# Optimization experiments

Hardware: AMD Instinct MI355X
Metric: run time of the kernel (lower is better)

## Reference

```python
import jax, jax.numpy as jnp
import numpy as np

EPS = 1e-5       # BatchNorm2d eps
NHEAD = 8
FILL = -1e30     # stands in for scores_fill_value=-inf (finite for grad safety)


def _proj(x, w, b, g, beta, mean, var):
    # Conv2d 1x1 over NCHW (H=1) == channel matmul, followed by eval-mode BatchNorm2d.
    y = jnp.einsum('oc,bcht->boht', w, x) + b[None, :, None, None]
    inv = g * jax.lax.rsqrt(var + EPS)
    return y * inv[None, :, None, None] + (beta - mean * inv)[None, :, None, None]


def setup_inputs() -> dict:
    rng = jax.random.key(0)
    ks = jax.random.split(rng, 10)
    B, C, T = 8, 512, 1024
    query = jax.random.normal(ks[0], (B, C, 1, T), jnp.float32)
    key = jax.random.normal(ks[1], (B, C, 1, T), jnp.float32)
    value = jax.random.normal(ks[2], (B, C, 1, T), jnp.float32)
    mask = jax.random.randint(ks[3], (B, 1, T, T), 0, 2).astype(jnp.int32)
    Ws = jax.random.normal(ks[4], (4, C, C), jnp.float32) * (1.0 / np.sqrt(C))
    bs = jax.random.normal(ks[5], (4, C), jnp.float32) * 0.1
    gammas = jax.random.uniform(ks[6], (4, C), jnp.float32, 0.5, 1.5)
    betas = jax.random.normal(ks[7], (4, C), jnp.float32) * 0.1
    means = jax.random.normal(ks[8], (4, C), jnp.float32) * 0.1
    vars_ = jax.random.uniform(ks[9], (4, C), jnp.float32, 0.5, 1.5)
    return dict(query=query, key=key, value=value, mask=mask, Ws=Ws, bs=bs,
                gammas=gammas, betas=betas, means=means, vars_=vars_)


def reference(query, key, value, mask, Ws, bs, gammas, betas, means, vars_):
    B, C, _, T1 = query.shape
    T2 = key.shape[3]
    h = NHEAD
    d_k = C // h
    denom = 1.0 / np.sqrt(d_k)

    q = _proj(query, Ws[0], bs[0], gammas[0], betas[0], means[0], vars_[0]).reshape(B, h, d_k, T1)
    k = _proj(key,   Ws[1], bs[1], gammas[1], betas[1], means[1], vars_[1]).reshape(B, h, d_k, T2)
    v = _proj(value, Ws[2], bs[2], gammas[2], betas[2], means[2], vars_[2]).reshape(B, h, d_k, T2)

    # scores = k^T @ q -> (B, h, T2, T1); softmax over key axis (dim=2, matching torch)
    scores = jnp.einsum('bhds,bhdt->bhst', k, q) * denom
    mask0 = jnp.transpose(mask, (0, 1, 3, 2)) == 0  # (B, 1, T2, T1)
    scores = jnp.where(mask0, FILL, scores)
    attn = jax.nn.softmax(scores, axis=2)
    attn = jnp.where(mask0, 0.0, attn)

    # x = v @ attn -> (B, h, d_k, T1) -> (B, C, 1, T1)
    x = jnp.einsum('bhds,bhst->bhdt', v, attn).reshape(B, C, 1, T1)
    out = _proj(x, Ws[3], bs[3], gammas[3], betas[3], means[3], vars_[3])

    # cache=None branch: new_cache = cat(raw key, raw value) along channel dim
    new_cache = jnp.concatenate([key, value], axis=1)
    return (out, new_cache)
```

## Files before the change

kernel.cpp:

```cpp
#include <hip/hip_runtime.h>

typedef unsigned short u16;
typedef unsigned int   u32;
typedef short  bfrag   __attribute__((ext_vector_type(8)));
typedef float  accfrag __attribute__((ext_vector_type(16)));
typedef unsigned int   u32x4 __attribute__((ext_vector_type(4)));
typedef unsigned short u16x4 __attribute__((ext_vector_type(4)));
typedef float          f32x4 __attribute__((ext_vector_type(4)));

#define B_SZ 8
#define C_SZ 512
#define T_SZ 1024
#define NH   8
#define DK   64

#define QSCL 0.18033688f

__device__ __forceinline__ u16 f2bf(float f) {
  u32 u = __float_as_uint(f);
  u = u + 0x7fffu + ((u >> 16) & 1u);
  return (u16)(u >> 16);
}

__device__ __forceinline__ float fexp2(float x) {
  return __builtin_amdgcn_exp2f(x);
}

__device__ __forceinline__ u32 cvtpk(float lo, float hi) {
  u32 r;
  asm("v_cvt_pk_bf16_f32 %0, %1, %2" : "=v"(r) : "v"(lo), "v"(hi));
  return r;
}

__device__ __forceinline__ void permswap(u32 &a, u32 &b) {
  asm volatile("v_permlane32_swap_b32 %0, %1" : "+v"(a), "+v"(b));
}

__device__ __forceinline__ void gload16(const u16* g, u16* l) {
  __builtin_amdgcn_global_load_lds(
      (const __attribute__((address_space(1))) void*)g,
      (__attribute__((address_space(3))) void*)l, 16, 0, 0);
}

__global__ void prep_w(const float* __restrict__ Ws, const float* __restrict__ gam,
                       const float* __restrict__ var, u16* __restrict__ Wp) {
  int idx = blockIdx.x * 256 + threadIdx.x;
  int io = idx >> 9;
  float inv = gam[io] * rsqrtf(var[io] + 1e-5f);
  Wp[idx] = f2bf(Ws[idx] * inv);
}

__global__ void prep_b(const float* __restrict__ bs, const float* __restrict__ gam,
                       const float* __restrict__ beta, const float* __restrict__ mean,
                       const float* __restrict__ var, float* __restrict__ bp) {
  int idx = blockIdx.x * 256 + threadIdx.x;
  float inv = gam[idx] * rsqrtf(var[idx] + 1e-5f);
  bp[idx] = bs[idx] * inv + beta[idx] - mean[idx] * inv;
}

__global__ void transpose_cvt(const float* __restrict__ q, const float* __restrict__ k,
                              const float* __restrict__ v, u16* __restrict__ Xt,
                              float* __restrict__ cache) {
  __shared__ float tile[32][33];
  int z = blockIdx.z;
  int src = z >> 3, b = z & 7;
  const float* in = (src == 0) ? q : ((src == 1) ? k : v);
  u16* out = Xt + (size_t)src * ((size_t)B_SZ * T_SZ * C_SZ);
  int t0 = blockIdx.x * 32, c0 = blockIdx.y * 32;
  int tx = threadIdx.x & 31, ty = threadIdx.x >> 5;
#pragma unroll
  for (int rr = 0; rr < 4; ++rr) {
    int c = c0 + ty + rr * 8;
    float val = in[(((size_t)b * C_SZ + c) << 10) + t0 + tx];
    tile[ty + rr * 8][tx] = val;
    if (src >= 1) {
      int cc = c + (src == 2 ? 512 : 0);
      cache[((size_t)b << 20) + ((size_t)cc << 10) + t0 + tx] = val;
    }
  }
  __syncthreads();
#pragma unroll
  for (int rr = 0; rr < 4; ++rr) {
    int t = t0 + ty + rr * 8;
    out[(((size_t)b << 10) + t) * C_SZ + c0 + tx] = f2bf(tile[tx][ty + rr * 8]);
  }
}

__global__ void mask_bits(const int* __restrict__ mask, u32* __restrict__ mbT) {
  int w = blockIdx.x * 256 + threadIdx.x;
  int bt = w >> 5;
  int st = w & 31;
  const int* mrow = mask + ((size_t)bt << 10) + (st << 5);
  u32 word = 0;
#pragma unroll
  for (int j = 0; j < 32; j += 4) {
    int4 m4 = *(const int4*)(mrow + j);
    word |= (m4.x != 0 ? 1u : 0u) << j;
    word |= (m4.y != 0 ? 1u : 0u) << (j + 1);
    word |= (m4.z != 0 ? 1u : 0u) << (j + 2);
    word |= (m4.w != 0 ? 1u : 0u) << (j + 3);
  }
  int b = bt >> 10, t = bt & 1023;
  mbT[(((size_t)b * 32 + st) << 10) + t] = word;
}

__launch_bounds__(256, 2)
__global__ void gemm_qkv(const u16* __restrict__ Wp, const float* __restrict__ bpA,
                         const u16* __restrict__ Xt,
                         u16* __restrict__ Qf, u16* __restrict__ Kf, u16* __restrict__ Vf) {
  __shared__ __align__(16) u16 lds[2 * 128 * 64];
  int tid = threadIdx.x;
  int src = blockIdx.z >> 3;
  int b   = blockIdx.z & 7;
  int t0 = blockIdx.x * 128;
  int o0 = blockIdx.y * 128;
  int wid = tid >> 6, lane = tid & 63;
  int ln = lane & 31, hi = lane >> 5;
  int wr = wid >> 1, wc = wid & 1;

  const u16* Wsrc = Wp + (size_t)src * 262144;
  const float* bp = bpA + src * 512;
  const u16* Xin  = Xt + (size_t)src * ((size_t)B_SZ * T_SZ * C_SZ);
  u16* Yout = (src == 0) ? Qf : (src == 1 ? Kf : Vf);

  const char* Ag = (const char*)Wsrc;
  const char* Bg = (const char*)(Xin + (((size_t)b << 10) + t0) * C_SZ);
  char* ldsA = (char*)lds;
  char* ldsB = (char*)lds + 16384;

  accfrag acc[2][2];
#pragma unroll
  for (int m2 = 0; m2 < 2; ++m2)
#pragma unroll
    for (int n2 = 0; n2 < 2; ++n2)
#pragma unroll
      for (int e = 0; e < 16; ++e) acc[m2][n2][e] = 0.f;

  int lin = tid * 16;
  for (int kt = 0; kt < 8; ++kt) {
    u32x4 ra[4], rb[4];
#pragma unroll
    for (int it = 0; it < 4; ++it) {
      int off = lin + it * 4096;
      int r = off >> 7, cb = off & 127;
      ra[it] = *(const u32x4*)(Ag + (size_t)(o0 + r) * 1024 + kt * 128 + cb);
      rb[it] = *(const u32x4*)(Bg + (size_t)r * 1024 + kt * 128 + cb);
    }
    __syncthreads();
#pragma unroll
    for (int it = 0; it < 4; ++it) {
      int off = lin + it * 4096;
      *(u32x4*)(ldsA + off) = ra[it];
      *(u32x4*)(ldsB + off) = rb[it];
    }
    __syncthreads();
#pragma unroll
    for (int kk = 0; kk < 4; ++kk) {
      bfrag a[2], bb[2];
#pragma unroll
      for (int m2 = 0; m2 < 2; ++m2)
        a[m2] = *(const bfrag*)(ldsA + (wr * 64 + m2 * 32 + ln) * 128 + kk * 32 + hi * 16);
#pragma unroll
      for (int n2 = 0; n2 < 2; ++n2)
        bb[n2] = *(const bfrag*)(ldsB + (wc * 64 + n2 * 32 + ln) * 128 + kk * 32 + hi * 16);
#pragma unroll
      for (int m2 = 0; m2 < 2; ++m2)
#pragma unroll
        for (int n2 = 0; n2 < 2; ++n2)
          acc[m2][n2] = __builtin_amdgcn_mfma_f32_32x32x16_bf16(a[m2], bb[n2], acc[m2][n2], 0, 0, 0);
    }
  }

  float oscl = (src == 0) ? QSCL : 1.0f;
#pragma unroll
  for (int m2 = 0; m2 < 2; ++m2) {
    int obase = o0 + wr * 64 + m2 * 32;
#pragma unroll
    for (int n2 = 0; n2 < 2; ++n2) {
      int t = t0 + wc * 64 + n2 * 32 + ln;
      if (src < 2) {
        int tt5 = t & 31, st = t >> 5;
#pragma unroll
        for (int g = 0; g < 4; ++g) {
          int d0 = obase + 8 * g + 4 * hi;
          int hh = d0 >> 6, dd = d0 & 63;
          u16x4 pk4;
#pragma unroll
          for (int qq = 0; qq < 4; ++qq)
            pk4[qq] = f2bf((acc[m2][n2][4 * g + qq] + bp[d0 + qq]) * oscl);
          size_t a = ((((size_t)b * 8 + hh) * 32 + st) << 11)
                   + (size_t)((dd >> 4) * 512 + (tt5 + 32 * ((dd >> 3) & 1)) * 8 + (dd & 7));
          *(u16x4*)(Yout + a) = pk4;
        }
      } else {
        int s = t, st = s >> 5;
#pragma unroll
        for (int r = 0; r < 16; ++r) {
          int d = obase + (r & 3) + 8 * (r >> 2) + 4 * hi;
          int hh = d >> 6, dd = d & 63;
          int fi = ((s >> 4) & 1) * 2 + ((dd >> 5) & 1);
          int l  = (dd & 31) + ((s >> 3) & 1) * 32;
          Yout[((((size_t)b * 8 + hh) * 32 + st) << 11)
               + (size_t)(fi * 512 + l * 8 + (s & 7))] = f2bf(acc[m2][n2][r] + bp[d]);
        }
      }
    }
  }
}

__launch_bounds__(256, 2)
__global__ void gemm_out(const u16* __restrict__ Wp, const float* __restrict__ bp,
                         const u16* __restrict__ Xin, float* __restrict__ Yout) {
  __shared__ __align__(16) u16 lds[2 * 128 * 64];
  int tid = threadIdx.x;
  int b  = blockIdx.z;
  int t0 = blockIdx.x * 128;
  int o0 = blockIdx.y * 128;
  int wid = tid >> 6, lane = tid & 63;
  int ln = lane & 31, hi = lane >> 5;
  int wr = wid >> 1, wc = wid & 1;

  const char* Ag = (const char*)Wp;
  const char* Bg = (const char*)(Xin + (((size_t)b << 10) + t0) * C_SZ);
  char* ldsA = (char*)lds;
  char* ldsB = (char*)lds + 16384;

  accfrag acc[2][2];
#pragma unroll
  for (int m2 = 0; m2 < 2; ++m2)
#pragma unroll
    for (int n2 = 0; n2 < 2; ++n2)
#pragma unroll
      for (int e = 0; e < 16; ++e) acc[m2][n2][e] = 0.f;

  int lin = tid * 16;
  for (int kt = 0; kt < 8; ++kt) {
    u32x4 ra[4], rb[4];
#pragma unroll
    for (int it = 0; it < 4; ++it) {
      int off = lin + it * 4096;
      int r = off >> 7, cb = off & 127;
      ra[it] = *(const u32x4*)(Ag + (size_t)(o0 + r) * 1024 + kt * 128 + cb);
      rb[it] = *(const u32x4*)(Bg + (size_t)r * 1024 + kt * 128 + cb);
    }
    __syncthreads();
#pragma unroll
    for (int it = 0; it < 4; ++it) {
      int off = lin + it * 4096;
      *(u32x4*)(ldsA + off) = ra[it];
      *(u32x4*)(ldsB + off) = rb[it];
    }
    __syncthreads();
#pragma unroll
    for (int kk = 0; kk < 4; ++kk) {
      bfrag a[2], bb[2];
#pragma unroll
      for (int m2 = 0; m2 < 2; ++m2)
        a[m2] = *(const bfrag*)(ldsA + (wr * 64 + m2 * 32 + ln) * 128 + kk * 32 + hi * 16);
#pragma unroll
      for (int n2 = 0; n2 < 2; ++n2)
        bb[n2] = *(const bfrag*)(ldsB + (wc * 64 + n2 * 32 + ln) * 128 + kk * 32 + hi * 16);
#pragma unroll
      for (int m2 = 0; m2 < 2; ++m2)
#pragma unroll
        for (int n2 = 0; n2 < 2; ++n2)
          acc[m2][n2] = __builtin_amdgcn_mfma_f32_32x32x16_bf16(a[m2], bb[n2], acc[m2][n2], 0, 0, 0);
    }
  }

#pragma unroll
  for (int m2 = 0; m2 < 2; ++m2) {
    int obase = o0 + wr * 64 + m2 * 32;
#pragma unroll
    for (int n2 = 0; n2 < 2; ++n2) {
      int t = t0 + wc * 64 + n2 * 32 + ln;
#pragma unroll
      for (int r = 0; r < 16; ++r) {
        int o = obase + (r & 3) + 8 * (r >> 2) + 4 * hi;
        Yout[(((size_t)b * C_SZ + o) << 10) + t] = acc[m2][n2][r] + bp[o];
      }
    }
  }
}

__launch_bounds__(512, 4)
__global__ void attn_fused(const u16* __restrict__ Qf, const u16* __restrict__ Kf,
                           const u16* __restrict__ Vf, const u32* __restrict__ mbT,
                           u16* __restrict__ X2) {
  __shared__ __align__(16) char smem[33 * 1024];
  u16*   sK   = (u16*)smem;
  u16*   sV   = (u16*)(smem + 16384);
  float* comb = (float*)smem;
  float* mlb  = (float*)(smem + 32768);

  int n = blockIdx.x;
  int bh = n & 63, tb = n >> 6;
  int b = bh >> 3, h = bh & 7;
  int tid = threadIdx.x;
  int wid = tid >> 6, lane = tid & 63;
  int grp = wid >> 2, wl = wid & 3;
  int ln = lane & 31, hi = lane >> 5;
  int tt = tb * 4 + wl;
  int t  = tt * 32 + ln;

  const u16* QfT = Qf + (((size_t)bh * 32 + tt) << 11);
  bfrag qf[4];
#pragma unroll
  for (int j = 0; j < 4; ++j)
    qf[j] = *(const bfrag*)(QfT + j * 512 + lane * 8);

  const u16* KfB = Kf + ((size_t)bh << 16);
  const u16* VfB = Vf + ((size_t)bh << 16);
  const u32* mcol = mbT + ((size_t)b << 15) + t;

  float m_run = -1.0e4f, l_run = 0.f;
  accfrag accd[2];
#pragma unroll
  for (int m2 = 0; m2 < 2; ++m2)
#pragma unroll
    for (int e = 0; e < 16; ++e) accd[m2][e] = 0.f;

  int gtid = tid & 255;
  int soff = gtid * 8;
  u16* sKg = sK + grp * 4096;
  u16* sVg = sV + grp * 4096;
  int st0 = grp * 16;

  gload16(KfB + ((size_t)st0 << 11) + soff, sKg + soff);
  gload16(VfB + ((size_t)st0 << 11) + soff, sVg + soff);
  u32 mw = mcol[st0 << 10];
  __syncthreads();

#pragma unroll 2
  for (int it = 0; it < 16; ++it) {
    int cur = it & 1, nxt = cur ^ 1;
    int st = st0 + it;
    u32 mn = 0;
    if (it < 15) {
      size_t tn = (size_t)(st + 1) << 11;
      gload16(KfB + tn + soff, sKg + nxt * 2048 + soff);
      gload16(VfB + tn + soff, sVg + nxt * 2048 + soff);
      mn = mcol[(st + 1) << 10];
    }

    bfrag kf[4], vf[4];
#pragma unroll
    for (int j = 0; j < 4; ++j) {
      kf[j] = *(const bfrag*)(sKg + cur * 2048 + j * 512 + lane * 8);
      vf[j] = *(const bfrag*)(sVg + cur * 2048 + j * 512 + lane * 8);
    }

    accfrag S;
#pragma unroll
    for (int e = 0; e < 16; ++e) S[e] = 0.f;
#pragma unroll
    for (int j = 0; j < 4; ++j)
      S = __builtin_amdgcn_mfma_f32_32x32x16_bf16(kf[j], qf[j], S, 0, 0, 0);

    u32 mbits = mw >> (4 * hi);
    float p[16];
#pragma unroll
    for (int r = 0; r < 16; ++r) {
      int pos = (r & 3) + 8 * (r >> 2);
      p[r] = ((mbits >> pos) & 1u) ? S[r] : -1e30f;
    }
    float q8[8], q4[4];
#pragma unroll
    for (int r = 0; r < 8; ++r) q8[r] = fmaxf(p[r], p[r + 8]);
#pragma unroll
    for (int r = 0; r < 4; ++r) q4[r] = fmaxf(q8[r], q8[r + 4]);
    float pmax = fmaxf(fmaxf(q4[0], q4[1]), fmaxf(q4[2], q4[3]));
    pmax = fmaxf(pmax, __shfl_xor(pmax, 32));

    if (__any(pmax > m_run + 11.5f)) {
      float m_new = fmaxf(m_run, pmax);
      float alpha = fexp2(m_run - m_new);
      l_run *= alpha;
#pragma unroll
      for (int m2 = 0; m2 < 2; ++m2)
#pragma unroll
        for (int e = 0; e < 16; ++e) accd[m2][e] *= alpha;
      m_run = m_new;
    }

#pragma unroll
    for (int r = 0; r < 16; ++r)
      p[r] = fexp2(p[r] - m_run);
    float s8[8], s4[4];
#pragma unroll
    for (int r = 0; r < 8; ++r) s8[r] = p[r] + p[r + 8];
#pragma unroll
    for (int r = 0; r < 4; ++r) s4[r] = s8[r] + s8[r + 4];
    float psum = (s4[0] + s4[1]) + (s4[2] + s4[3]);
    psum += __shfl_xor(psum, 32);
    l_run += psum;

    bfrag pf[2];
#pragma unroll
    for (int j2 = 0; j2 < 2; ++j2) {
      u32 A0 = cvtpk(p[8 * j2 + 0], p[8 * j2 + 1]);
      u32 A1 = cvtpk(p[8 * j2 + 2], p[8 * j2 + 3]);
      u32 B0 = cvtpk(p[8 * j2 + 4], p[8 * j2 + 5]);
      u32 B1 = cvtpk(p[8 * j2 + 6], p[8 * j2 + 7]);
      permswap(A0, B0);
      permswap(A1, B1);
      union { u32 u[4]; bfrag f; } pu;
      pu.u[0] = A0; pu.u[1] = A1; pu.u[2] = B0; pu.u[3] = B1;
      pf[j2] = pu.f;
    }
#pragma unroll
    for (int j2 = 0; j2 < 2; ++j2)
#pragma unroll
      for (int m2 = 0; m2 < 2; ++m2)
        accd[m2] = __builtin_amdgcn_mfma_f32_32x32x16_bf16(vf[j2 * 2 + m2], pf[j2], accd[m2], 0, 0, 0);

    __syncthreads();
    mw = mn;
  }

  if (grp == 1) {
#pragma unroll
    for (int m2 = 0; m2 < 2; ++m2)
#pragma unroll
      for (int e = 0; e < 16; ++e)
        comb[wl * 2048 + (m2 * 16 + e) * 64 + lane] = accd[m2][e];
    if (hi == 0) {
      mlb[(wl * 32 + ln) * 2]     = m_run;
      mlb[(wl * 32 + ln) * 2 + 1] = l_run;
    }
  }
  __syncthreads();
  if (grp == 0) {
    float m1v = mlb[(wl * 32 + ln) * 2];
    float l1v = mlb[(wl * 32 + ln) * 2 + 1];
    float M  = fmaxf(m_run, m1v);
    float w0 = fexp2(m_run - M), w1 = fexp2(m1v - M);
    float l  = l_run * w0 + l1v * w1;
    float invl = (l > 0.f) ? 1.f / l : 0.f;
    u16* Orow = X2 + (((size_t)b << 10) + t) * C_SZ + h * DK;
#pragma unroll
    for (int m2 = 0; m2 < 2; ++m2)
#pragma unroll
      for (int g = 0; g < 4; ++g) {
        u16x4 pk4;
#pragma unroll
        for (int qq = 0; qq < 4; ++qq) {
          int e = 4 * g + qq;
          float v2 = comb[wl * 2048 + (m2 * 16 + e) * 64 + lane];
          pk4[qq] = f2bf((accd[m2][e] * w0 + v2 * w1) * invl);
        }
        *(u16x4*)(Orow + m2 * 32 + 8 * g + 4 * hi) = pk4;
      }
  }
}

extern "C" void kernel_launch(void* const* d_in, const int* in_sizes, int n_in,
                              void* d_out, int out_size, void* d_ws, size_t ws_size,
                              hipStream_t stream) {
  (void)in_sizes; (void)n_in; (void)out_size; (void)ws_size;
  const float* q    = (const float*)d_in[0];
  const float* k    = (const float*)d_in[1];
  const float* v    = (const float*)d_in[2];
  const int*   mask = (const int*)d_in[3];
  const float* Ws   = (const float*)d_in[4];
  const float* bs   = (const float*)d_in[5];
  const float* gam  = (const float*)d_in[6];
  const float* beta = (const float*)d_in[7];
  const float* mean = (const float*)d_in[8];
  const float* var  = (const float*)d_in[9];

  float* out   = (float*)d_out;
  float* cache = out + (size_t)B_SZ * C_SZ * T_SZ;

  const size_t ARR = (size_t)B_SZ * T_SZ * C_SZ;
  char* ws = (char*)d_ws;
  u16*   Wp = (u16*)(ws);
  float* bp = (float*)(ws + 2097152);
  u16*   Xt = (u16*)(ws + 2162688);
  u16*   Qt = Xt + 3 * ARR;
  u16*   Kt = Qt + ARR;
  u16*   Vb = Kt + ARR;
  u16*   X2 = Vb + ARR;
  u32*   mb = (u32*)((char*)(X2 + ARR));

  prep_w<<<4096, 256, 0, stream>>>(Ws, gam, var, Wp);
  prep_b<<<8, 256, 0, stream>>>(bs, gam, beta, mean, var, bp);
  transpose_cvt<<<dim3(32, 16, 24), 256, 0, stream>>>(q, k, v, Xt, cache);
  mask_bits<<<1024, 256, 0, stream>>>(mask, mb);

  gemm_qkv<<<dim3(8, 4, 24), 256, 0, stream>>>(Wp, bp, Xt, Qt, Kt, Vb);
  attn_fused<<<512, 512, 0, stream>>>(Qt, Kt, Vb, mb, X2);
  gemm_out<<<dim3(8, 4, 8), 256, 0, stream>>>(Wp + 786432, bp + 1536, X2, out);
}
```

Before: 115.5 us.

## Prefetch next K-tile into registers and XOR-swizzle LDS in projection GEMMs

Both projection GEMM kernels now load the next K-slice from global memory into registers while MFMAs run on the current slice, overlapping global latency with compute. LDS stores and fragment reads use an XOR swizzle on the 16-byte column chunk keyed by row, to cut bank conflicts on the 128-byte-stride row reads. Register pressure rises slightly, and the number of barriers per iteration is unchanged.

```diff
diff --git a/kernel.cpp b/kernel.cpp
--- a/kernel.cpp
+++ b/kernel.cpp
@@ -137,32 +137,44 @@
       for (int e = 0; e < 16; ++e) acc[m2][n2][e] = 0.f;
 
   int lin = tid * 16;
+  u32x4 ra[4], rb[4];
+#pragma unroll
+  for (int it = 0; it < 4; ++it) {
+    int off = lin + it * 4096;
+    int r = off >> 7, cb = off & 127;
+    ra[it] = *(const u32x4*)(Ag + (size_t)(o0 + r) * 1024 + cb);
+    rb[it] = *(const u32x4*)(Bg + (size_t)r * 1024 + cb);
+  }
+
   for (int kt = 0; kt < 8; ++kt) {
-    u32x4 ra[4], rb[4];
+    __syncthreads();
 #pragma unroll
     for (int it = 0; it < 4; ++it) {
       int off = lin + it * 4096;
-      int r = off >> 7, cb = off & 127;
-      ra[it] = *(const u32x4*)(Ag + (size_t)(o0 + r) * 1024 + kt * 128 + cb);
-      rb[it] = *(const u32x4*)(Bg + (size_t)r * 1024 + kt * 128 + cb);
+      int swz = off ^ (((off >> 7) & 7) << 4);
+      *(u32x4*)(ldsA + swz) = ra[it];
+      *(u32x4*)(ldsB + swz) = rb[it];
     }
     __syncthreads();
-#pragma unroll
-    for (int it = 0; it < 4; ++it) {
-      int off = lin + it * 4096;
-      *(u32x4*)(ldsA + off) = ra[it];
-      *(u32x4*)(ldsB + off) = rb[it];
-    }
-    __syncthreads();
+    if (kt < 7) {
+#pragma unroll
+      for (int it = 0; it < 4; ++it) {
+        int off = lin + it * 4096;
+        int r = off >> 7, cb = off & 127;
+        ra[it] = *(const u32x4*)(Ag + (size_t)(o0 + r) * 1024 + (kt + 1) * 128 + cb);
+        rb[it] = *(const u32x4*)(Bg + (size_t)r * 1024 + (kt + 1) * 128 + cb);
+      }
+    }
 #pragma unroll
     for (int kk = 0; kk < 4; ++kk) {
+      int csw = (kk * 32 + hi * 16) ^ ((ln & 7) << 4);
       bfrag a[2], bb[2];
 #pragma unroll
       for (int m2 = 0; m2 < 2; ++m2)
-        a[m2] = *(const bfrag*)(ldsA + (wr * 64 + m2 * 32 + ln) * 128 + kk * 32 + hi * 16);
+        a[m2] = *(const bfrag*)(ldsA + (wr * 64 + m2 * 32 + ln) * 128 + csw);
 #pragma unroll
       for (int n2 = 0; n2 < 2; ++n2)
-        bb[n2] = *(const bfrag*)(ldsB + (wc * 64 + n2 * 32 + ln) * 128 + kk * 32 + hi * 16);
+        bb[n2] = *(const bfrag*)(ldsB + (wc * 64 + n2 * 32 + ln) * 128 + csw);
 #pragma unroll
       for (int m2 = 0; m2 < 2; ++m2)
 #pragma unroll
@@ -234,32 +246,44 @@
       for (int e = 0; e < 16; ++e) acc[m2][n2][e] = 0.f;
 
   int lin = tid * 16;
+  u32x4 ra[4], rb[4];
+#pragma unroll
+  for (int it = 0; it < 4; ++it) {
+    int off = lin + it * 4096;
+    int r = off >> 7, cb = off & 127;
+    ra[it] = *(const u32x4*)(Ag + (size_t)(o0 + r) * 1024 + cb);
+    rb[it] = *(const u32x4*)(Bg + (size_t)r * 1024 + cb);
+  }
+
   for (int kt = 0; kt < 8; ++kt) {
-    u32x4 ra[4], rb[4];
+    __syncthreads();
 #pragma unroll
     for (int it = 0; it < 4; ++it) {
       int off = lin + it * 4096;
-      int r = off >> 7, cb = off & 127;
-      ra[it] = *(const u32x4*)(Ag + (size_t)(o0 + r) * 1024 + kt * 128 + cb);
-      rb[it] = *(const u32x4*)(Bg + (size_t)r * 1024 + kt * 128 + cb);
+      int swz = off ^ (((off >> 7) & 7) << 4);
+      *(u32x4*)(ldsA + swz) = ra[it];
+      *(u32x4*)(ldsB + swz) = rb[it];
     }
     __syncthreads();
-#pragma unroll
-    for (int it = 0; it < 4; ++it) {
-      int off = lin + it * 4096;
-      *(u32x4*)(ldsA + off) = ra[it];
-      *(u32x4*)(ldsB + off) = rb[it];
-    }
-    __syncthreads();
+    if (kt < 7) {
+#pragma unroll
+      for (int it = 0; it < 4; ++it) {
+        int off = lin + it * 4096;
+        int r = off >> 7, cb = off & 127;
+        ra[it] = *(const u32x4*)(Ag + (size_t)(o0 + r) * 1024 + (kt + 1) * 128 + cb);
+        rb[it] = *(const u32x4*)(Bg + (size_t)r * 1024 + (kt + 1) * 128 + cb);
+      }
+    }
 #pragma unroll
     for (int kk = 0; kk < 4; ++kk) {
+      int csw = (kk * 32 + hi * 16) ^ ((ln & 7) << 4);
       bfrag a[2], bb[2];
 #pragma unroll
       for (int m2 = 0; m2 < 2; ++m2)
-        a[m2] = *(const bfrag*)(ldsA + (wr * 64 + m2 * 32 + ln) * 128 + kk * 32 + hi * 16);
+        a[m2] = *(const bfrag*)(ldsA + (wr * 64 + m2 * 32 + ln) * 128 + csw);
 #pragma unroll
       for (int n2 = 0; n2 < 2; ++n2)
-        bb[n2] = *(const bfrag*)(ldsB + (wc * 64 + n2 * 32 + ln) * 128 + kk * 32 + hi * 16);
+        bb[n2] = *(const bfrag*)(ldsB + (wc * 64 + n2 * 32 + ln) * 128 + csw);
 #pragma unroll
       for (int m2 = 0; m2 < 2; ++m2)
 #pragma unroll
```

Result: faster. 97.63 us (-15.5%).

## Double-buffer GEMM tiles with async LDS loads; split attention keys across four groups

Applied to the files above, without the earlier changes.

Both projection GEMMs now stage tiles straight from global memory into LDS with gload16 into a double buffer, prefetching the next k-tile while the current one is computed, and drop one barrier per iteration. The attention kernel switches from 2 key-split groups of 4 waves to 4 groups of 2 waves, which doubles the grid to 1024 blocks. It also removes its K/V double-buffer prefetch and merges partial softmax states in a two-level tree reduction through LDS. This trades more blocks and parallelism against extra combine steps and no overlap of loads in the attention loop. GEMM LDS use doubles to 64KB per block, which may limit occupancy.

```diff
diff --git a/kernel.cpp b/kernel.cpp
--- a/kernel.cpp
+++ b/kernel.cpp
@@ -108,7 +108,7 @@
 __global__ void gemm_qkv(const u16* __restrict__ Wp, const float* __restrict__ bpA,
                          const u16* __restrict__ Xt,
                          u16* __restrict__ Qf, u16* __restrict__ Kf, u16* __restrict__ Vf) {
-  __shared__ __align__(16) u16 lds[2 * 128 * 64];
+  __shared__ __align__(16) u16 lds[32768];
   int tid = threadIdx.x;
   int src = blockIdx.z >> 3;
   int b   = blockIdx.z & 7;
@@ -125,8 +125,7 @@
 
   const char* Ag = (const char*)Wsrc;
   const char* Bg = (const char*)(Xin + (((size_t)b << 10) + t0) * C_SZ);
-  char* ldsA = (char*)lds;
-  char* ldsB = (char*)lds + 16384;
+  char* ldsc = (char*)lds;
 
   accfrag acc[2][2];
 #pragma unroll
@@ -137,32 +136,34 @@
       for (int e = 0; e < 16; ++e) acc[m2][n2][e] = 0.f;
 
   int lin = tid * 16;
+
+#define STAGE_G(buf, kt) {                                                         \
+  _Pragma("unroll")                                                                \
+  for (int itx = 0; itx < 4; ++itx) {                                              \
+    int off = lin + itx * 4096;                                                    \
+    int r = off >> 7, cb = off & 127;                                              \
+    gload16((const u16*)(Ag + (size_t)(o0 + r) * 1024 + (kt) * 128 + cb),          \
+            (u16*)(ldsc + (buf) * 32768 + off));                                   \
+    gload16((const u16*)(Bg + (size_t)r * 1024 + (kt) * 128 + cb),                 \
+            (u16*)(ldsc + (buf) * 32768 + 16384 + off));                           \
+  } }
+
+  STAGE_G(0, 0);
+#pragma unroll 2
   for (int kt = 0; kt < 8; ++kt) {
-    u32x4 ra[4], rb[4];
-#pragma unroll
-    for (int it = 0; it < 4; ++it) {
-      int off = lin + it * 4096;
-      int r = off >> 7, cb = off & 127;
-      ra[it] = *(const u32x4*)(Ag + (size_t)(o0 + r) * 1024 + kt * 128 + cb);
-      rb[it] = *(const u32x4*)(Bg + (size_t)r * 1024 + kt * 128 + cb);
-    }
+    int cur = kt & 1;
     __syncthreads();
-#pragma unroll
-    for (int it = 0; it < 4; ++it) {
-      int off = lin + it * 4096;
-      *(u32x4*)(ldsA + off) = ra[it];
-      *(u32x4*)(ldsB + off) = rb[it];
-    }
-    __syncthreads();
+    if (kt < 7) STAGE_G(cur ^ 1, kt + 1);
 #pragma unroll
     for (int kk = 0; kk < 4; ++kk) {
+      int c = kk * 32 + hi * 16;
       bfrag a[2], bb[2];
 #pragma unroll
       for (int m2 = 0; m2 < 2; ++m2)
-        a[m2] = *(const bfrag*)(ldsA + (wr * 64 + m2 * 32 + ln) * 128 + kk * 32 + hi * 16);
+        a[m2] = *(const bfrag*)(ldsc + cur * 32768 + (wr * 64 + m2 * 32 + ln) * 128 + c);
 #pragma unroll
       for (int n2 = 0; n2 < 2; ++n2)
-        bb[n2] = *(const bfrag*)(ldsB + (wc * 64 + n2 * 32 + ln) * 128 + kk * 32 + hi * 16);
+        bb[n2] = *(const bfrag*)(ldsc + cur * 32768 + 16384 + (wc * 64 + n2 * 32 + ln) * 128 + c);
 #pragma unroll
       for (int m2 = 0; m2 < 2; ++m2)
 #pragma unroll
@@ -206,12 +207,13 @@
       }
     }
   }
+#undef STAGE_G
 }
 
 __launch_bounds__(256, 2)
 __global__ void gemm_out(const u16* __restrict__ Wp, const float* __restrict__ bp,
                          const u16* __restrict__ Xin, float* __restrict__ Yout) {
-  __shared__ __align__(16) u16 lds[2 * 128 * 64];
+  __shared__ __align__(16) u16 lds[32768];
   int tid = threadIdx.x;
   int b  = blockIdx.z;
   int t0 = blockIdx.x * 128;
@@ -222,8 +224,7 @@
 
   const char* Ag = (const char*)Wp;
   const char* Bg = (const char*)(Xin + (((size_t)b << 10) + t0) * C_SZ);
-  char* ldsA = (char*)lds;
-  char* ldsB = (char*)lds + 16384;
+  char* ldsc = (char*)lds;
 
   accfrag acc[2][2];
 #pragma unroll
@@ -234,32 +235,34 @@
       for (int e = 0; e < 16; ++e) acc[m2][n2][e] = 0.f;
 
   int lin = tid * 16;
+
+#define STAGE_G(buf, kt) {                                                         \
+  _Pragma("unroll")                                                                \
+  for (int itx = 0; itx < 4; ++itx) {                                              \
+    int off = lin + itx * 4096;                                                    \
+    int r = off >> 7, cb = off & 127;                                              \
+    gload16((const u16*)(Ag + (size_t)(o0 + r) * 1024 + (kt) * 128 + cb),          \
+            (u16*)(ldsc + (buf) * 32768 + off));                                   \
+    gload16((const u16*)(Bg + (size_t)r * 1024 + (kt) * 128 + cb),                 \
+            (u16*)(ldsc + (buf) * 32768 + 16384 + off));                           \
+  } }
+
+  STAGE_G(0, 0);
+#pragma unroll 2
   for (int kt = 0; kt < 8; ++kt) {
-    u32x4 ra[4], rb[4];
-#pragma unroll
-    for (int it = 0; it < 4; ++it) {
-      int off = lin + it * 4096;
-      int r = off >> 7, cb = off & 127;
-      ra[it] = *(const u32x4*)(Ag + (size_t)(o0 + r) * 1024 + kt * 128 + cb);
-      rb[it] = *(const u32x4*)(Bg + (size_t)r * 1024 + kt * 128 + cb);
-    }
+    int cur = kt & 1;
     __syncthreads();
-#pragma unroll
-    for (int it = 0; it < 4; ++it) {
-      int off = lin + it * 4096;
-      *(u32x4*)(ldsA + off) = ra[it];
-      *(u32x4*)(ldsB + off) = rb[it];
-    }
-    __syncthreads();
+    if (kt < 7) STAGE_G(cur ^ 1, kt + 1);
 #pragma unroll
     for (int kk = 0; kk < 4; ++kk) {
+      int c = kk * 32 + hi * 16;
       bfrag a[2], bb[2];
 #pragma unroll
       for (int m2 = 0; m2 < 2; ++m2)
-        a[m2] = *(const bfrag*)(ldsA + (wr * 64 + m2 * 32 + ln) * 128 + kk * 32 + hi * 16);
+        a[m2] = *(const bfrag*)(ldsc + cur * 32768 + (wr * 64 + m2 * 32 + ln) * 128 + c);
 #pragma unroll
       for (int n2 = 0; n2 < 2; ++n2)
-        bb[n2] = *(const bfrag*)(ldsB + (wc * 64 + n2 * 32 + ln) * 128 + kk * 32 + hi * 16);
+        bb[n2] = *(const bfrag*)(ldsc + cur * 32768 + 16384 + (wc * 64 + n2 * 32 + ln) * 128 + c);
 #pragma unroll
       for (int m2 = 0; m2 < 2; ++m2)
 #pragma unroll
@@ -281,26 +284,24 @@
       }
     }
   }
+#undef STAGE_G
 }
 
 __launch_bounds__(512, 4)
 __global__ void attn_fused(const u16* __restrict__ Qf, const u16* __restrict__ Kf,
                            const u16* __restrict__ Vf, const u32* __restrict__ mbT,
                            u16* __restrict__ X2) {
-  __shared__ __align__(16) char smem[33 * 1024];
-  u16*   sK   = (u16*)smem;
-  u16*   sV   = (u16*)(smem + 16384);
-  float* comb = (float*)smem;
-  float* mlb  = (float*)(smem + 32768);
+  __shared__ __align__(16) char smem[34816];
+  float* mlb = (float*)(smem + 32768);
 
   int n = blockIdx.x;
   int bh = n & 63, tb = n >> 6;
   int b = bh >> 3, h = bh & 7;
   int tid = threadIdx.x;
   int wid = tid >> 6, lane = tid & 63;
-  int grp = wid >> 2, wl = wid & 3;
+  int grp = wid >> 1, wl = wid & 1;
   int ln = lane & 31, hi = lane >> 5;
-  int tt = tb * 4 + wl;
+  int tt = tb * 2 + wl;
   int t  = tt * 32 + ln;
 
   const u16* QfT = Qf + (((size_t)bh * 32 + tt) << 11);
@@ -320,34 +321,28 @@
 #pragma unroll
     for (int e = 0; e < 16; ++e) accd[m2][e] = 0.f;
 
-  int gtid = tid & 255;
-  int soff = gtid * 8;
-  u16* sKg = sK + grp * 4096;
-  u16* sVg = sV + grp * 4096;
-  int st0 = grp * 16;
-
-  gload16(KfB + ((size_t)st0 << 11) + soff, sKg + soff);
-  gload16(VfB + ((size_t)st0 << 11) + soff, sVg + soff);
-  u32 mw = mcol[st0 << 10];
-  __syncthreads();
-
-#pragma unroll 2
-  for (int it = 0; it < 16; ++it) {
-    int cur = it & 1, nxt = cur ^ 1;
-    int st = st0 + it;
-    u32 mn = 0;
-    if (it < 15) {
-      size_t tn = (size_t)(st + 1) << 11;
-      gload16(KfB + tn + soff, sKg + nxt * 2048 + soff);
-      gload16(VfB + tn + soff, sVg + nxt * 2048 + soff);
-      mn = mcol[(st + 1) << 10];
-    }
+  int gid = tid & 127;
+  u16* sK = (u16*)smem + grp * 4096;
+  u16* sV = sK + 2048;
+
+  for (int it = 0; it < 8; ++it) {
+    int st = grp * 8 + it;
+    __syncthreads();
+    {
+      size_t tn = (size_t)st << 11;
+      gload16(KfB + tn + gid * 8,        sK + gid * 8);
+      gload16(KfB + tn + 1024 + gid * 8, sK + 1024 + gid * 8);
+      gload16(VfB + tn + gid * 8,        sV + gid * 8);
+      gload16(VfB + tn + 1024 + gid * 8, sV + 1024 + gid * 8);
+    }
+    u32 mw = mcol[st << 10];
+    __syncthreads();
 
     bfrag kf[4], vf[4];
 #pragma unroll
     for (int j = 0; j < 4; ++j) {
-      kf[j] = *(const bfrag*)(sKg + cur * 2048 + j * 512 + lane * 8);
-      vf[j] = *(const bfrag*)(sVg + cur * 2048 + j * 512 + lane * 8);
+      kf[j] = *(const bfrag*)(sK + j * 512 + lane * 8);
+      vf[j] = *(const bfrag*)(sV + j * 512 + lane * 8);
     }
 
     accfrag S;
@@ -413,29 +408,59 @@
 #pragma unroll
       for (int m2 = 0; m2 < 2; ++m2)
         accd[m2] = __builtin_amdgcn_mfma_f32_32x32x16_bf16(vf[j2 * 2 + m2], pf[j2], accd[m2], 0, 0, 0);
-
-    __syncthreads();
-    mw = mn;
-  }
-
-  if (grp == 1) {
+  }
+
+  float* comb = (float*)smem;
+  __syncthreads();
+  if (grp & 1) {
+    float* dst = comb + ((grp >> 1) * 4096 + wl * 2048);
 #pragma unroll
     for (int m2 = 0; m2 < 2; ++m2)
 #pragma unroll
       for (int e = 0; e < 16; ++e)
-        comb[wl * 2048 + (m2 * 16 + e) * 64 + lane] = accd[m2][e];
+        dst[(m2 * 16 + e) * 64 + lane] = accd[m2][e];
     if (hi == 0) {
-      mlb[(wl * 32 + ln) * 2]     = m_run;
-      mlb[(wl * 32 + ln) * 2 + 1] = l_run;
+      mlb[((grp * 2 + wl) * 32 + ln) * 2]     = m_run;
+      mlb[((grp * 2 + wl) * 32 + ln) * 2 + 1] = l_run;
+    }
+  }
+  __syncthreads();
+  if (!(grp & 1)) {
+    int pg = grp + 1;
+    const float* srcp = comb + ((pg >> 1) * 4096 + wl * 2048);
+    float m1 = mlb[((pg * 2 + wl) * 32 + ln) * 2];
+    float l1 = mlb[((pg * 2 + wl) * 32 + ln) * 2 + 1];
+    float M  = fmaxf(m_run, m1);
+    float w0 = fexp2(m_run - M), w1 = fexp2(m1 - M);
+    l_run = l_run * w0 + l1 * w1;
+    m_run = M;
+#pragma unroll
+    for (int m2 = 0; m2 < 2; ++m2)
+#pragma unroll
+      for (int e = 0; e < 16; ++e)
+        accd[m2][e] = accd[m2][e] * w0 + srcp[(m2 * 16 + e) * 64 + lane] * w1;
+  }
+  __syncthreads();
+  if (grp == 2) {
+    float* dst = comb + wl * 2048;
+#pragma unroll
+    for (int m2 = 0; m2 < 2; ++m2)
+#pragma unroll
+      for (int e = 0; e < 16; ++e)
+        dst[(m2 * 16 + e) * 64 + lane] = accd[m2][e];
+    if (hi == 0) {
+      mlb[((4 + wl) * 32 + ln) * 2]     = m_run;
+      mlb[((4 + wl) * 32 + ln) * 2 + 1] = l_run;
     }
   }
   __syncthreads();
   if (grp == 0) {
-    float m1v = mlb[(wl * 32 + ln) * 2];
-    float l1v = mlb[(wl * 32 + ln) * 2 + 1];
-    float M  = fmaxf(m_run, m1v);
-    float w0 = fexp2(m_run - M), w1 = fexp2(m1v - M);
-    float l  = l_run * w0 + l1v * w1;
+    const float* srcp = comb + wl * 2048;
+    float m1 = mlb[((4 + wl) * 32 + ln) * 2];
+    float l1 = mlb[((4 + wl) * 32 + ln) * 2 + 1];
+    float M  = fmaxf(m_run, m1);
+    float w0 = fexp2(m_run - M), w1 = fexp2(m1 - M);
+    float l  = l_run * w0 + l1 * w1;
     float invl = (l > 0.f) ? 1.f / l : 0.f;
     u16* Orow = X2 + (((size_t)b << 10) + t) * C_SZ + h * DK;
 #pragma unroll
@@ -446,7 +471,7 @@
 #pragma unroll
         for (int qq = 0; qq < 4; ++qq) {
           int e = 4 * g + qq;
-          float v2 = comb[wl * 2048 + (m2 * 16 + e) * 64 + lane];
+          float v2 = srcp[(m2 * 16 + e) * 64 + lane];
           pk4[qq] = f2bf((accd[m2][e] * w0 + v2 * w1) * invl);
         }
         *(u16x4*)(Orow + m2 * 32 + 8 * g + 4 * hi) = pk4;
@@ -489,6 +514,6 @@
   mask_bits<<<1024, 256, 0, stream>>>(mask, mb);
 
   gemm_qkv<<<dim3(8, 4, 24), 256, 0, stream>>>(Wp, bp, Xt, Qt, Kt, Vb);
-  attn_fused<<<512, 512, 0, stream>>>(Qt, Kt, Vb, mb, X2);
+  attn_fused<<<1024, 512, 0, stream>>>(Qt, Kt, Vb, mb, X2);
   gemm_out<<<dim3(8, 4, 8), 256, 0, stream>>>(Wp + 786432, bp + 1536, X2, out);
 }
```

Result: slower. 119.1 us (+3.1%).
